# Kernel optimization log

Hardware: AMD Instinct MI355X
Metric: run time of the kernel (lower is better)

Reference implementation:

```python
import jax, jax.numpy as jnp
import numpy as np

HIDDEN = 256
BATCH = 16
SEQ = 8192


def setup_inputs() -> dict:
    key = jax.random.key(0)
    k1, k2 = jax.random.split(key)
    x = jax.random.normal(k1, (BATCH, SEQ, HIDDEN), dtype=jnp.float32)
    # rotor_net parameters: Linear(hidden, hidden) followed by tanh
    W = jax.random.normal(k2, (HIDDEN, HIDDEN), dtype=jnp.float32) / np.sqrt(HIDDEN)
    b = jnp.zeros((HIDDEN,), dtype=jnp.float32)
    return {"x": x, "W": W, "b": b}


def reference(x, W, b):
    # Original torch code loops over subseq_size=10 chunks of the flattened
    # (B*S, H) tokens, applying rotor_net to each chunk and concatenating.
    # rotor_net is row-wise (Linear + tanh), so chunked application is
    # mathematically identical to one batched application over all tokens.
    B, S, H = x.shape
    flat = x.reshape(-1, H)                      # (B*S, H)
    out = jnp.tanh(flat @ W.T + b)               # (B*S, H)
    return out.reshape(B, S, -1)
```

## Files before the change

### kernel.cpp

```cpp
#include <hip/hip_runtime.h>
#include <hip/hip_bf16.h>


#define HIDDEN 256
#define M_TOTAL (16 * 8192)
#define NBLK 768
#define NSTREAM 384

using bf16x8 = __attribute__((ext_vector_type(8))) __bf16;
using f32x4  = __attribute__((ext_vector_type(4))) float;

__device__ __forceinline__ void gload16(const void* g, void* l) {
    __builtin_amdgcn_global_load_lds(
        (const __attribute__((address_space(1))) void*)g,
        (__attribute__((address_space(3))) void*)l, 16, 0, 0);
}

__global__ __launch_bounds__(256) void wfrag_kernel(const float* __restrict__ W,
                                                    __bf16* __restrict__ WF) {
    const int gid  = blockIdx.x * 256 + threadIdx.x;
    const int lane = gid & 63;
    const int t    = (gid >> 6) & 3;
    const int c    = (gid >> 8) & 7;
    const int nb   = gid >> 11;
    const int lr = lane & 15, q = lane >> 4;
    const float* src = W + (size_t)(nb * 64 + t * 16 + lr) * HIDDEN + c * 32 + q * 8;
    float4 lo = *(const float4*)src;
    float4 hi = *(const float4*)(src + 4);
    bf16x8 v;
    v[0] = (__bf16)lo.x; v[1] = (__bf16)lo.y; v[2] = (__bf16)lo.z; v[3] = (__bf16)lo.w;
    v[4] = (__bf16)hi.x; v[5] = (__bf16)hi.y; v[6] = (__bf16)hi.z; v[7] = (__bf16)hi.w;
    *(bf16x8*)(WF + (size_t)gid * 8) = v;
}

__global__ __launch_bounds__(256, 3) void rotor_kernel(const float* __restrict__ X,
                                                       const __bf16* __restrict__ WF,
                                                       const float* __restrict__ bias,
                                                       float* __restrict__ Y) {
    __shared__ __align__(16) float sX[3][16 * 256];

    const int tid  = threadIdx.x;
    const int lane = tid & 63;
    const int wave = tid >> 6;
    const int lr = lane & 15, q = lane >> 4;

    const int bid = blockIdx.x;
    const int xcd = bid & 7;
    const int sg  = bid >> 3;
    const int h   = sg & 1;
    const int st  = (sg >> 1) * 8 + xcd;
    const int nit = (st < 128) ? 22 : 21;

    const int nb  = h * 2 + (wave >> 1);
    const int tl0 = (wave & 1) * 2;
    const __bf16* wf = WF + (size_t)nb * (8 * 4 * 512) + lane * 8;
    bf16x8 bW[8][2];
#pragma unroll
    for (int c = 0; c < 8; ++c)
#pragma unroll
        for (int t = 0; t < 2; ++t)
            bW[c][t] = *(const bf16x8*)(wf + (c * 4 + tl0 + t) * 512);

    float bv[2];
#pragma unroll
    for (int t = 0; t < 2; ++t) bv[t] = bias[h * 128 + wave * 32 + t * 16 + lr];

    int srcoff[4];
#pragma unroll
    for (int k = 0; k < 4; ++k) {
        const int r = wave * 4 + k;
        srcoff[k] = (lane * 16) ^ (((r & 7) << 5) | ((r & 8) << 1));
    }
    const int swr = ((lr & 7) << 3) | ((lr & 8) >> 1);

#pragma unroll
    for (int p = 0; p < 2; ++p) {
        const int rc = st + p * NSTREAM;
#pragma unroll
        for (int k = 0; k < 4; ++k)
            gload16((const char*)X + (size_t)(rc * 16 + wave * 4 + k) * 1024 + srcoff[k],
                    (char*)&sX[p][(wave * 4 + k) * 256]);
    }
    asm volatile("s_waitcnt vmcnt(4)" ::: "memory");
    __builtin_amdgcn_s_barrier();
    asm volatile("" ::: "memory");

    int cur = 0;
#pragma unroll 1
    for (int it = 0; it < nit; ++it) {
        if (it + 2 < nit) {
            int b2 = cur + 2; if (b2 >= 3) b2 -= 3;
            const int rcn = st + (it + 2) * NSTREAM;
#pragma unroll
            for (int k = 0; k < 4; ++k)
                gload16((const char*)X + (size_t)(rcn * 16 + wave * 4 + k) * 1024 + srcoff[k],
                        (char*)&sX[b2][(wave * 4 + k) * 256]);
        }

        const int rc = st + it * NSTREAM;
        const float* sxr = &sX[cur][lr * 256];
        f32x4 acc0 = {0.f, 0.f, 0.f, 0.f};
        f32x4 acc1 = {0.f, 0.f, 0.f, 0.f};
#pragma unroll
        for (int c = 0; c < 8; ++c) {
            const int b0 = c * 32 + q * 8;
            f32x4 lo = *(const f32x4*)(sxr + (b0 ^ swr));
            f32x4 hi = *(const f32x4*)(sxr + ((b0 + 4) ^ swr));
            bf16x8 a;
            a[0] = (__bf16)lo[0]; a[1] = (__bf16)lo[1];
            a[2] = (__bf16)lo[2]; a[3] = (__bf16)lo[3];
            a[4] = (__bf16)hi[0]; a[5] = (__bf16)hi[1];
            a[6] = (__bf16)hi[2]; a[7] = (__bf16)hi[3];
            acc0 = __builtin_amdgcn_mfma_f32_16x16x32_bf16(a, bW[c][0], acc0, 0, 0, 0);
            acc1 = __builtin_amdgcn_mfma_f32_16x16x32_bf16(a, bW[c][1], acc1, 0, 0, 0);
        }

        float* yb = Y + (size_t)(rc * 16 + q * 4) * HIDDEN + h * 128 + wave * 32 + lr;
#pragma unroll
        for (int t = 0; t < 2; ++t)
#pragma unroll
            for (int i = 0; i < 4; ++i) {
                float z = (t ? acc1[i] : acc0[i]) + bv[t];
                z = fminf(fmaxf(z, -10.f), 10.f);
                const float e2 = __expf(2.0f * z);
                yb[(size_t)i * HIDDEN + t * 16] = __fdividef(e2 - 1.0f, e2 + 1.0f);
            }

        asm volatile("s_waitcnt vmcnt(12)" ::: "memory");
        __builtin_amdgcn_s_barrier();
        asm volatile("" ::: "memory");
        cur = (cur == 2) ? 0 : cur + 1;
    }
}

extern "C" void kernel_launch(void* const* d_in, const int* in_sizes, int n_in,
                              void* d_out, int out_size, void* d_ws, size_t ws_size,
                              hipStream_t stream) {
    const float* X    = (const float*)d_in[0];
    const float* W    = (const float*)d_in[1];
    const float* bias = (const float*)d_in[2];
    float* Y          = (float*)d_out;
    __bf16* WF        = (__bf16*)d_ws;

    wfrag_kernel<<<dim3(32), dim3(256), 0, stream>>>(W, WF);
    rotor_kernel<<<dim3(NBLK), dim3(256), 0, stream>>>(X, WF, bias, Y);
}
```

Before: 245.9 us.

## Switch to 32x32 MFMA tiles with register-staged bf16 LDS double buffer

The kernel now processes 32-row chunks with 32x32x16 bf16 MFMA instead of 16-row chunks with two 16x16x32 MFMAs per step. X is loaded into registers one chunk ahead, converted to bf16 once, and written to a double-buffered bf16 LDS tile, replacing the triple-buffered fp32 global_load_lds path. This halves LDS footprint and cuts per-wave conversion work. In exchange it adds register pressure for the prefetched X, and the fp32-to-bf16 conversion now sits in the main loop before the barrier.

```diff
diff --git a/kernel.cpp b/kernel.cpp
--- a/kernel.cpp
+++ b/kernel.cpp
@@ -6,130 +6,119 @@
 #define M_TOTAL (16 * 8192)
 #define NBLK 768
 #define NSTREAM 384
+#define NCHUNK 4096
 
-using bf16x8 = __attribute__((ext_vector_type(8))) __bf16;
-using f32x4  = __attribute__((ext_vector_type(4))) float;
+using bf16x8  = __attribute__((ext_vector_type(8))) __bf16;
+using f32x4   = __attribute__((ext_vector_type(4))) float;
+using f32x16  = __attribute__((ext_vector_type(16))) float;
 
-__device__ __forceinline__ void gload16(const void* g, void* l) {
-    __builtin_amdgcn_global_load_lds(
-        (const __attribute__((address_space(1))) void*)g,
-        (__attribute__((address_space(3))) void*)l, 16, 0, 0);
+__device__ __forceinline__ bf16x8 cvt8(float4 a, float4 b) {
+    bf16x8 v;
+    v[0] = (__bf16)a.x; v[1] = (__bf16)a.y; v[2] = (__bf16)a.z; v[3] = (__bf16)a.w;
+    v[4] = (__bf16)b.x; v[5] = (__bf16)b.y; v[6] = (__bf16)b.z; v[7] = (__bf16)b.w;
+    return v;
 }
 
 __global__ __launch_bounds__(256) void wfrag_kernel(const float* __restrict__ W,
                                                     __bf16* __restrict__ WF) {
     const int gid  = blockIdx.x * 256 + threadIdx.x;
     const int lane = gid & 63;
-    const int t    = (gid >> 6) & 3;
-    const int c    = (gid >> 8) & 7;
-    const int nb   = gid >> 11;
-    const int lr = lane & 15, q = lane >> 4;
-    const float* src = W + (size_t)(nb * 64 + t * 16 + lr) * HIDDEN + c * 32 + q * 8;
+    const int kf   = (gid >> 6) & 15;
+    const int g    = gid >> 10;
+    const float* src = W + (size_t)(g * 32 + (lane & 31)) * HIDDEN
+                         + kf * 16 + (lane >> 5) * 8;
     float4 lo = *(const float4*)src;
     float4 hi = *(const float4*)(src + 4);
-    bf16x8 v;
-    v[0] = (__bf16)lo.x; v[1] = (__bf16)lo.y; v[2] = (__bf16)lo.z; v[3] = (__bf16)lo.w;
-    v[4] = (__bf16)hi.x; v[5] = (__bf16)hi.y; v[6] = (__bf16)hi.z; v[7] = (__bf16)hi.w;
-    *(bf16x8*)(WF + (size_t)gid * 8) = v;
+    *(bf16x8*)(WF + (size_t)gid * 8) = cvt8(lo, hi);
 }
 
 __global__ __launch_bounds__(256, 3) void rotor_kernel(const float* __restrict__ X,
                                                        const __bf16* __restrict__ WF,
                                                        const float* __restrict__ bias,
                                                        float* __restrict__ Y) {
-    __shared__ __align__(16) float sX[3][16 * 256];
+    __shared__ __align__(16) __bf16 sA[2][8192];
 
     const int tid  = threadIdx.x;
     const int lane = tid & 63;
     const int wave = tid >> 6;
-    const int lr = lane & 15, q = lane >> 4;
+    const int col  = lane & 31;
+    const int hi   = lane >> 5;
 
     const int bid = blockIdx.x;
     const int xcd = bid & 7;
     const int sg  = bid >> 3;
     const int h   = sg & 1;
     const int st  = (sg >> 1) * 8 + xcd;
-    const int nit = (st < 128) ? 22 : 21;
+    const int nit = (st < 256) ? 11 : 10;
 
-    const int nb  = h * 2 + (wave >> 1);
-    const int tl0 = (wave & 1) * 2;
-    const __bf16* wf = WF + (size_t)nb * (8 * 4 * 512) + lane * 8;
-    bf16x8 bW[8][2];
+    const __bf16* wf = WF + (size_t)(h * 4 + wave) * 8192 + lane * 8;
+    bf16x8 bW[16];
 #pragma unroll
-    for (int c = 0; c < 8; ++c)
+    for (int kf = 0; kf < 16; ++kf)
+        bW[kf] = *(const bf16x8*)(wf + kf * 512);
+
+    const float bv = bias[h * 128 + wave * 32 + col];
+
+    const int r  = tid >> 3;
+    const int c0 = tid & 7;
+    const int wo = c0 * 1024 + r * 8;
+    const float* xcol = X + (size_t)r * HIDDEN + c0 * 32;
+
+    float4 xr[8];
+    auto loadx = [&](int rc) {
+        const float* xs = xcol + (size_t)rc * 32 * HIDDEN;
 #pragma unroll
-        for (int t = 0; t < 2; ++t)
-            bW[c][t] = *(const bf16x8*)(wf + (c * 4 + tl0 + t) * 512);
+        for (int i = 0; i < 8; ++i) xr[i] = *(const float4*)(xs + i * 4);
+    };
+    auto stage = [&](__bf16* sbuf) {
+        bf16x8 v0 = cvt8(xr[0], xr[1]);
+        bf16x8 v1 = cvt8(xr[2], xr[3]);
+        bf16x8 v2 = cvt8(xr[4], xr[5]);
+        bf16x8 v3 = cvt8(xr[6], xr[7]);
+        *(bf16x8*)(sbuf + wo)       = v0;
+        *(bf16x8*)(sbuf + wo + 256) = v1;
+        *(bf16x8*)(sbuf + wo + 512) = v2;
+        *(bf16x8*)(sbuf + wo + 768) = v3;
+    };
 
-    float bv[2];
-#pragma unroll
-    for (int t = 0; t < 2; ++t) bv[t] = bias[h * 128 + wave * 32 + t * 16 + lr];
-
-    int srcoff[4];
-#pragma unroll
-    for (int k = 0; k < 4; ++k) {
-        const int r = wave * 4 + k;
-        srcoff[k] = (lane * 16) ^ (((r & 7) << 5) | ((r & 8) << 1));
-    }
-    const int swr = ((lr & 7) << 3) | ((lr & 8) >> 1);
-
-#pragma unroll
-    for (int p = 0; p < 2; ++p) {
-        const int rc = st + p * NSTREAM;
-#pragma unroll
-        for (int k = 0; k < 4; ++k)
-            gload16((const char*)X + (size_t)(rc * 16 + wave * 4 + k) * 1024 + srcoff[k],
-                    (char*)&sX[p][(wave * 4 + k) * 256]);
-    }
-    asm volatile("s_waitcnt vmcnt(4)" ::: "memory");
+    loadx(st);
+    stage(&sA[0][0]);
+    loadx(st + NSTREAM);
+    asm volatile("s_waitcnt lgkmcnt(0)" ::: "memory");
     __builtin_amdgcn_s_barrier();
     asm volatile("" ::: "memory");
 
-    int cur = 0;
 #pragma unroll 1
     for (int it = 0; it < nit; ++it) {
-        if (it + 2 < nit) {
-            int b2 = cur + 2; if (b2 >= 3) b2 -= 3;
-            const int rcn = st + (it + 2) * NSTREAM;
+        if (it + 1 < nit) stage(&sA[(it + 1) & 1][0]);
+
+        if (it + 2 < nit) loadx(st + (it + 2) * NSTREAM);
+
+        const __bf16* ab = &sA[it & 1][lane * 8];
+        f32x16 acc = {0.f, 0.f, 0.f, 0.f, 0.f, 0.f, 0.f, 0.f,
+                      0.f, 0.f, 0.f, 0.f, 0.f, 0.f, 0.f, 0.f};
 #pragma unroll
-            for (int k = 0; k < 4; ++k)
-                gload16((const char*)X + (size_t)(rcn * 16 + wave * 4 + k) * 1024 + srcoff[k],
-                        (char*)&sX[b2][(wave * 4 + k) * 256]);
+        for (int kf = 0; kf < 16; ++kf) {
+            bf16x8 a = *(const bf16x8*)(ab + kf * 512);
+            acc = __builtin_amdgcn_mfma_f32_32x32x16_bf16(a, bW[kf], acc, 0, 0, 0);
         }
 
         const int rc = st + it * NSTREAM;
-        const float* sxr = &sX[cur][lr * 256];
-        f32x4 acc0 = {0.f, 0.f, 0.f, 0.f};
-        f32x4 acc1 = {0.f, 0.f, 0.f, 0.f};
+        float* yb = Y + (size_t)rc * 32 * HIDDEN + h * 128 + wave * 32 + col;
 #pragma unroll
-        for (int c = 0; c < 8; ++c) {
-            const int b0 = c * 32 + q * 8;
-            f32x4 lo = *(const f32x4*)(sxr + (b0 ^ swr));
-            f32x4 hi = *(const f32x4*)(sxr + ((b0 + 4) ^ swr));
-            bf16x8 a;
-            a[0] = (__bf16)lo[0]; a[1] = (__bf16)lo[1];
-            a[2] = (__bf16)lo[2]; a[3] = (__bf16)lo[3];
-            a[4] = (__bf16)hi[0]; a[5] = (__bf16)hi[1];
-            a[6] = (__bf16)hi[2]; a[7] = (__bf16)hi[3];
-            acc0 = __builtin_amdgcn_mfma_f32_16x16x32_bf16(a, bW[c][0], acc0, 0, 0, 0);
-            acc1 = __builtin_amdgcn_mfma_f32_16x16x32_bf16(a, bW[c][1], acc1, 0, 0, 0);
-        }
-
-        float* yb = Y + (size_t)(rc * 16 + q * 4) * HIDDEN + h * 128 + wave * 32 + lr;
+        for (int g2 = 0; g2 < 4; ++g2)
 #pragma unroll
-        for (int t = 0; t < 2; ++t)
-#pragma unroll
-            for (int i = 0; i < 4; ++i) {
-                float z = (t ? acc1[i] : acc0[i]) + bv[t];
+            for (int rr = 0; rr < 4; ++rr) {
+                const int row = rr + 8 * g2 + 4 * hi;
+                float z = acc[g2 * 4 + rr] + bv;
                 z = fminf(fmaxf(z, -10.f), 10.f);
                 const float e2 = __expf(2.0f * z);
-                yb[(size_t)i * HIDDEN + t * 16] = __fdividef(e2 - 1.0f, e2 + 1.0f);
+                yb[(size_t)row * HIDDEN] = __fdividef(e2 - 1.0f, e2 + 1.0f);
             }
 
-        asm volatile("s_waitcnt vmcnt(12)" ::: "memory");
+        asm volatile("s_waitcnt lgkmcnt(0)" ::: "memory");
         __builtin_amdgcn_s_barrier();
         asm volatile("" ::: "memory");
-        cur = (cur == 2) ? 0 : cur + 1;
     }
 }
 
```

Measured after the change: 242.7 us. Within noise of the previous version (-1.3%).
